# Kernel optimization log

Hardware: AMD Instinct MI355X
Metric: run time of the kernel (lower is better)

Reference implementation:

```python
import jax, jax.numpy as jnp
import numpy as np

HIDDEN_DIM = 2048
NUM_HEADS = 16
HEAD_DIM = HIDDEN_DIM // NUM_HEADS


def setup_inputs() -> dict:
    key = jax.random.key(0)
    k1, k2, k3 = jax.random.split(key, 3)
    x = jax.random.normal(k1, (2, 2048, HIDDEN_DIM), dtype=jnp.float32)
    # nn.Linear weight layout is [out, in]; we store transposed [in, out] for x @ W
    W_qkv = jax.random.normal(k2, (HIDDEN_DIM, 3 * HIDDEN_DIM), dtype=jnp.float32) * (HIDDEN_DIM ** -0.5)
    W_out = jax.random.normal(k3, (HIDDEN_DIM, HIDDEN_DIM), dtype=jnp.float32) * (HIDDEN_DIM ** -0.5)
    return {"x": x, "W_qkv": W_qkv, "W_out": W_out}


def reference(x, W_qkv, W_out):
    B, T, D = x.shape
    H, Hd = NUM_HEADS, HEAD_DIM
    qkv = (x @ W_qkv).reshape(B, T, 3, H, Hd)
    q = qkv[:, :, 0].transpose(0, 2, 1, 3)  # [B,H,T,Hd]
    k = qkv[:, :, 1].transpose(0, 2, 1, 3)
    v = qkv[:, :, 2].transpose(0, 2, 1, 3)
    scale = 1.0 / jnp.sqrt(jnp.asarray(Hd, dtype=x.dtype))
    attn = jnp.einsum('bhqd,bhkd->bhqk', q, k) * scale  # [B,H,T,T]
    causal = jnp.tril(jnp.ones((T, T), dtype=bool))
    attn = jnp.where(causal, attn, jnp.asarray(-jnp.inf, dtype=attn.dtype))
    attn = jax.nn.softmax(attn, axis=-1)
    out = jnp.einsum('bhqk,bhkd->bhqd', attn, v)  # [B,H,T,Hd]
    out = out.transpose(0, 2, 1, 3).reshape(B, T, D)
    return out @ W_out
```

## Files before the change

kernel.cpp:

```cpp
#include <hip/hip_runtime.h>


typedef unsigned short ushort;
typedef __attribute__((ext_vector_type(8))) short short8;
typedef __attribute__((ext_vector_type(4))) float floatx4;

#define T_SEQ 2048
#define NQKV  6144
#define DMODEL 2048
#define HDIM  128
#define NEG_BIG (-3.0e38f)

__device__ __forceinline__ ushort f2bf(float f) {
  unsigned u = __float_as_uint(f);
  u += 0x7fffu + ((u >> 16) & 1u);
  return (ushort)(u >> 16);
}
__device__ __forceinline__ void stout(ushort* p, float v) { *p = f2bf(v); }
__device__ __forceinline__ void stout(float* p, float v)  { *p = v; }

__device__ __forceinline__ void gload_lds16(const ushort* g, ushort* l) {
  __builtin_amdgcn_global_load_lds(
      (const __attribute__((address_space(1))) void*)g,
      (__attribute__((address_space(3))) void*)l,
      16, 0, 0);
}

__global__ void cvt2d(const float* __restrict__ in, ushort* __restrict__ out,
                      int R, int C, int ld_in) {
  int idx = blockIdx.x * blockDim.x + threadIdx.x;
  int c4 = C >> 2;
  if (idx >= R * c4) return;
  int r = idx / c4, c = (idx - r * c4) * 4;
  float4 v = *(const float4*)(in + (size_t)r * ld_in + c);
  ushort4 o;
  o.x = f2bf(v.x); o.y = f2bf(v.y); o.z = f2bf(v.z); o.w = f2bf(v.w);
  *(ushort4*)(out + (size_t)r * C + c) = o;
}

__global__ void cvt2dT(const float* __restrict__ in, ushort* __restrict__ out,
                       int R, int C, int ld_in) {
  __shared__ float tile[32][33];
  int c0 = blockIdx.x * 32, r0 = blockIdx.y * 32;
  int tx = threadIdx.x, ty = threadIdx.y;
#pragma unroll
  for (int q = 0; q < 4; q++)
    tile[ty + q * 8][tx] = in[(size_t)(r0 + ty + q * 8) * ld_in + c0 + tx];
  __syncthreads();
#pragma unroll
  for (int q = 0; q < 4; q++)
    out[(size_t)(c0 + ty + q * 8) * R + r0 + tx] = f2bf(tile[tx][ty + q * 8]);
}

template <typename OutT>
__global__ void gemm_bt(
    const ushort* __restrict__ A, const ushort* __restrict__ Bt,
    OutT* __restrict__ C, int M, int N, int K, int ldc) {
  __shared__ ushort sA[128 * 32];
  __shared__ ushort sB[128 * 32];
  const int tid = threadIdx.x;
  const int w = tid >> 6, l = tid & 63;
  const int quad = l >> 4, l16 = l & 15;
  const int row0 = blockIdx.x * 128, col0 = blockIdx.y * 128;
  const int wm = (w >> 1) * 64, wn = (w & 1) * 64;

  floatx4 acc[4][4];
  const floatx4 zero = {0.f, 0.f, 0.f, 0.f};
#pragma unroll
  for (int i = 0; i < 4; i++)
#pragma unroll
    for (int j = 0; j < 4; j++) acc[i][j] = zero;

  const int srow = w * 16 + (l >> 2);
  const int scol = (l & 3) * 8;
  const ushort* gA = A + (size_t)(row0 + srow) * K + scol;
  const ushort* gB = Bt + (size_t)(col0 + srow) * K + scol;
  ushort* lA = &sA[(w * 16) * 32];
  ushort* lB = &sB[(w * 16) * 32];

  for (int k0 = 0; k0 < K; k0 += 32) {
    __syncthreads();
    gload_lds16(gA + k0, lA);
    gload_lds16(gA + k0 + (size_t)64 * K, lA + 64 * 32);
    gload_lds16(gB + k0, lB);
    gload_lds16(gB + k0 + (size_t)64 * K, lB + 64 * 32);
    __syncthreads();
    short8 af[4], bfr[4];
#pragma unroll
    for (int i = 0; i < 4; i++)
      af[i] = *(const short8*)&sA[(wm + i * 16 + l16) * 32 + quad * 8];
#pragma unroll
    for (int j = 0; j < 4; j++)
      bfr[j] = *(const short8*)&sB[(wn + j * 16 + l16) * 32 + quad * 8];
#pragma unroll
    for (int i = 0; i < 4; i++)
#pragma unroll
      for (int j = 0; j < 4; j++)
        acc[i][j] = __builtin_amdgcn_mfma_f32_16x16x32_bf16(af[i], bfr[j], acc[i][j], 0, 0, 0);
  }

#pragma unroll
  for (int i = 0; i < 4; i++)
#pragma unroll
    for (int j = 0; j < 4; j++) {
      int r0 = row0 + wm + i * 16 + quad * 4;
      int c = col0 + wn + j * 16 + l16;
#pragma unroll
      for (int r = 0; r < 4; r++)
        stout(&C[(size_t)(r0 + r) * ldc + c], acc[i][j][r]);
    }
}

__global__ __launch_bounds__(256, 2) void flash_attn(
    const ushort* __restrict__ qkv, ushort* __restrict__ attn) {
  __shared__ ushort sK[2][16 * 528];
  __shared__ ushort sVt[128 * 72];
  __shared__ ushort sP[4 * 16 * 72];

  const int tid = threadIdx.x;
  const int w = tid >> 6, l = tid & 63;
  const int quad = l >> 4, l16 = l & 15;
  const int bh = blockIdx.x;
  const int qt = 31 - (int)blockIdx.y;
  const int b = bh >> 4, h = bh & 15;
  const size_t rowbase = (size_t)b * T_SEQ;

  short8 qf[4];
  {
    const ushort* qp = qkv + (rowbase + qt * 64 + w * 16 + l16) * NQKV + h * HDIM + quad * 8;
#pragma unroll
    for (int s = 0; s < 4; s++) qf[s] = *(const short8*)(qp + s * 32);
  }
  floatx4 o[8];
  const floatx4 zero = {0.f, 0.f, 0.f, 0.f};
#pragma unroll
  for (int n = 0; n < 8; n++) o[n] = zero;
  float m_i[4], l_i[4];
#pragma unroll
  for (int r = 0; r < 4; r++) { m_i[r] = NEG_BIG; l_i[r] = 0.f; }

  const ushort* gK = qkv + (rowbase + w * 16 + (l >> 4)) * NQKV + 2048 + h * HDIM + (l & 15) * 8;
  auto issueK = [&](int kt, int buf) {
#pragma unroll
    for (int c = 0; c < 4; c++)
      gload_lds16(gK + (size_t)(kt * 64 + c * 4) * NQKV, &sK[buf][(w * 4 + c) * 528]);
  };
  const int v_hd0 = (tid & 15) * 8;
  const int v_t0 = 2 * (tid >> 4);
  const ushort* gV = qkv + rowbase * NQKV + 4096 + h * HDIM + v_hd0;
  short8 vcur[4], vnxt[4];
  auto loadV = [&](int kt, short8* dst) {
#pragma unroll
    for (int c = 0; c < 2; c++) {
      const ushort* g = gV + (size_t)(kt * 64 + v_t0 + 32 * c) * NQKV;
      dst[c] = *(const short8*)g;
      dst[2 + c] = *(const short8*)(g + NQKV);
    }
  };

  ushort* myP = &sP[w * 16 * 72];
  const float scale = 0.08838834764831845f;

  auto attn_step = [&](bool diag, int buf) {
    floatx4 S[4];
#pragma unroll
    for (int j = 0; j < 4; j++) S[j] = zero;
#pragma unroll
    for (int s = 0; s < 4; s++)
#pragma unroll
      for (int j = 0; j < 4; j++) {
        int row = j * 16 + l16;
        short8 kf = *(const short8*)&sK[buf][(row >> 2) * 528 + (row & 3) * 128 + s * 32 + quad * 8];
        S[j] = __builtin_amdgcn_mfma_f32_16x16x32_bf16(qf[s], kf, S[j], 0, 0, 0);
      }
#pragma unroll
    for (int j = 0; j < 4; j++)
#pragma unroll
      for (int r = 0; r < 4; r++) {
        float v = S[j][r] * scale;
        if (diag && (j * 16 + l16 > w * 16 + quad * 4 + r)) v = NEG_BIG;
        S[j][r] = v;
      }
    float alpha[4];
#pragma unroll
    for (int r = 0; r < 4; r++) {
      float v = fmaxf(fmaxf(S[0][r], S[1][r]), fmaxf(S[2][r], S[3][r]));
      v = fmaxf(v, __shfl_xor(v, 1, 16));
      v = fmaxf(v, __shfl_xor(v, 2, 16));
      v = fmaxf(v, __shfl_xor(v, 4, 16));
      v = fmaxf(v, __shfl_xor(v, 8, 16));
      float mn = fmaxf(m_i[r], v);
      alpha[r] = __expf(m_i[r] - mn);
      m_i[r] = mn;
    }
#pragma unroll
    for (int j = 0; j < 4; j++)
#pragma unroll
      for (int r = 0; r < 4; r++) S[j][r] = __expf(S[j][r] - m_i[r]);
#pragma unroll
    for (int r = 0; r < 4; r++)
      l_i[r] = l_i[r] * alpha[r] + S[0][r] + S[1][r] + S[2][r] + S[3][r];
#pragma unroll
    for (int n = 0; n < 8; n++)
#pragma unroll
      for (int r = 0; r < 4; r++) o[n][r] *= alpha[r];
#pragma unroll
    for (int j = 0; j < 4; j++)
#pragma unroll
      for (int r = 0; r < 4; r++)
        myP[(quad * 4 + r) * 72 + j * 16 + l16] = f2bf(S[j][r]);
#pragma unroll
    for (int s = 0; s < 2; s++) {
      short8 pf = *(const short8*)&myP[l16 * 72 + s * 32 + quad * 8];
#pragma unroll
      for (int n = 0; n < 8; n++) {
        int hd = n * 16 + l16;
        short8 vf = *(const short8*)&sVt[hd * 72 + 8 * ((s * 4 + quad) ^ ((hd >> 3) & 7))];
        o[n] = __builtin_amdgcn_mfma_f32_16x16x32_bf16(pf, vf, o[n], 0, 0, 0);
      }
    }
  };

  issueK(0, 0);
  loadV(0, vcur);
  for (int kt = 0; kt <= qt; kt++) {
    const int buf = kt & 1;
    __syncthreads();
#pragma unroll
    for (int c = 0; c < 2; c++) {
      int tw = (v_t0 >> 1) + 16 * c;
#pragma unroll
      for (int j = 0; j < 8; j++) {
        int hd = v_hd0 + j;
        int phys = hd * 72 + 2 * (tw & 3) + 8 * ((tw >> 2) ^ ((hd >> 3) & 7));
        unsigned pv = ((unsigned)(ushort)vcur[c][j]) | (((unsigned)(ushort)vcur[2 + c][j]) << 16);
        *(unsigned*)&sVt[phys] = pv;
      }
    }
    __syncthreads();
    if (kt < qt) {
      issueK(kt + 1, buf ^ 1);
      loadV(kt + 1, vnxt);
    }
    attn_step(kt == qt, buf);
    if (kt < qt) {
#pragma unroll
      for (int c = 0; c < 4; c++) vcur[c] = vnxt[c];
    }
  }

#pragma unroll
  for (int r = 0; r < 4; r++) {
    float v = l_i[r];
    v += __shfl_xor(v, 1, 16);
    v += __shfl_xor(v, 2, 16);
    v += __shfl_xor(v, 4, 16);
    v += __shfl_xor(v, 8, 16);
    l_i[r] = 1.0f / v;
  }
#pragma unroll
  for (int n = 0; n < 8; n++) {
    int col = h * HDIM + n * 16 + l16;
#pragma unroll
    for (int r = 0; r < 4; r++) {
      int row = qt * 64 + w * 16 + quad * 4 + r;
      attn[(rowbase + row) * DMODEL + col] = f2bf(o[n][r] * l_i[r]);
    }
  }
}

extern "C" void kernel_launch(void* const* d_in, const int* in_sizes, int n_in,
                              void* d_out, int out_size, void* d_ws, size_t ws_size,
                              hipStream_t stream) {
  const float* xf    = (const float*)d_in[0];
  const float* Wqkvf = (const float*)d_in[1];
  const float* Woutf = (const float*)d_in[2];
  float* outf = (float*)d_out;
  char* ws = (char*)d_ws;

  const size_t SZ_QKV  = (size_t)4096 * 6144 * 2;
  const size_t SZ_ATTN = (size_t)4096 * 2048 * 2;
  const size_t SZ_WQT  = (size_t)6144 * 2048 * 2;

  ushort* xb = (ushort*)d_out;
  cvt2d<<<8192, 256, 0, stream>>>(xf, xb, 4096, 2048, 2048);

  if (ws_size >= SZ_QKV + SZ_ATTN + SZ_WQT) {
    ushort* qkv   = (ushort*)ws;
    ushort* attnb = (ushort*)(ws + SZ_QKV);
    ushort* WT    = (ushort*)(ws + SZ_QKV + SZ_ATTN);
    cvt2dT<<<dim3(192, 64), dim3(32, 8), 0, stream>>>(Wqkvf, WT, 2048, 6144, NQKV);
    gemm_bt<ushort><<<dim3(32, 48), 256, 0, stream>>>(xb, WT, qkv, 4096, 6144, 2048, NQKV);
    flash_attn<<<dim3(32, 32), 256, 0, stream>>>(qkv, attnb);
    cvt2dT<<<dim3(64, 64), dim3(32, 8), 0, stream>>>(Woutf, WT, 2048, 2048, 2048);
    gemm_bt<float><<<dim3(32, 16), 256, 0, stream>>>(attnb, WT, outf, 4096, 2048, 2048, DMODEL);
  } else {
    ushort* qkv   = (ushort*)ws;
    float*  of    = (float*)ws;
    ushort* wbT   = (ushort*)d_out + (size_t)4096 * 2048;
    ushort* attnb = xb;
    for (int s = 0; s < 3; s++) {
      cvt2dT<<<dim3(64, 64), dim3(32, 8), 0, stream>>>(Wqkvf + s * 2048, wbT, 2048, 2048, NQKV);
      gemm_bt<ushort><<<dim3(32, 16), 256, 0, stream>>>(xb, wbT, qkv + s * 2048, 4096, 2048, 2048, NQKV);
    }
    flash_attn<<<dim3(32, 32), 256, 0, stream>>>(qkv, attnb);
    cvt2dT<<<dim3(64, 64), dim3(32, 8), 0, stream>>>(Woutf, wbT, 2048, 2048, 2048);
    gemm_bt<float><<<dim3(32, 16), 256, 0, stream>>>(attnb, wbT, of, 4096, 2048, 2048, DMODEL);
    hipMemcpyAsync(outf, of, (size_t)4096 * 2048 * 4, hipMemcpyDeviceToDevice, stream);
  }
}
```

Measured before the change: 395.0 us.

## Add 256x256-tile pipelined GEMM with async LDS loads for QKV projection

Adds a new GEMM kernel with 256x256 output tiles, 8 waves per block and direct global-to-LDS loads. It double-buffers K-steps and splits them into phases that interleave the next stage loads with MFMA work, using explicit waitcnt, barriers and setprio. The QKV projection now uses this kernel to raise data reuse per tile and hide load latency. The larger tiles give only 384 blocks and raise register and LDS pressure, and the hand-written waitcnt counts must match the issued loads exactly.

```diff
diff --git a/kernel.cpp b/kernel.cpp
--- a/kernel.cpp
+++ b/kernel.cpp
@@ -10,6 +10,9 @@
 #define DMODEL 2048
 #define HDIM  128
 #define NEG_BIG (-3.0e38f)
+
+#define WAITVM(n) asm volatile("s_waitcnt vmcnt(" #n ")" ::: "memory")
+#define WAITLGKM0 asm volatile("s_waitcnt lgkmcnt(0)" ::: "memory")
 
 __device__ __forceinline__ ushort f2bf(float f) {
   unsigned u = __float_as_uint(f);
@@ -111,6 +114,99 @@
     }
 }
 
+template <typename OutT>
+__global__ __launch_bounds__(512, 2) void gemm_bt_256(
+    const ushort* __restrict__ A, const ushort* __restrict__ Bt,
+    OutT* __restrict__ C, int M, int N, int K, int ldc) {
+  __shared__ ushort sA[2][2][256 * 32];
+  __shared__ ushort sB[2][2][256 * 32];
+  const int tid = threadIdx.x;
+  const int wid = tid >> 6, l = tid & 63;
+  const int quad = l >> 4, l16 = l & 15;
+  const int wr = wid >> 2, wc = wid & 3;
+  const int row0 = blockIdx.x * 256, col0 = blockIdx.y * 256;
+  const int NT = K >> 6;
+
+  floatx4 acc[8][4];
+  const floatx4 zero = {0.f, 0.f, 0.f, 0.f};
+#pragma unroll
+  for (int i = 0; i < 8; i++)
+#pragma unroll
+    for (int j = 0; j < 4; j++) acc[i][j] = zero;
+
+  const ushort* gA = A + (size_t)(row0 + wid * 32 + (l >> 2)) * K + (l & 3) * 8;
+  const ushort* gB = Bt + (size_t)(col0 + wid * 32 + (l >> 2)) * K + (l & 3) * 8;
+
+  auto stageA = [&](int tt, int ks) {
+    ushort* dst = &sA[tt & 1][ks][(wid * 32) * 32];
+    const ushort* g = gA + (size_t)tt * 64 + ks * 32;
+    gload_lds16(g, dst);
+    gload_lds16(g + (size_t)16 * K, dst + 16 * 32);
+  };
+  auto stageB = [&](int tt, int ks) {
+    ushort* dst = &sB[tt & 1][ks][(wid * 32) * 32];
+    const ushort* g = gB + (size_t)tt * 64 + ks * 32;
+    gload_lds16(g, dst);
+    gload_lds16(g + (size_t)16 * K, dst + 16 * 32);
+  };
+
+  stageA(0, 0); stageB(0, 0); stageA(0, 1); stageB(0, 1);
+  if (NT > 1) {
+    stageA(1, 0); stageB(1, 0);
+    WAITVM(4);
+  } else {
+    WAITVM(0);
+  }
+  __builtin_amdgcn_s_barrier();
+
+#define PHASE(ks, ch, STAGE_STMT, VM_TAIL)                                    \
+  {                                                                           \
+    if ((ch) == 0) {                                                          \
+      _Pragma("unroll")                                                       \
+      for (int j = 0; j < 4; j++)                                             \
+        bfr[j] = *(const short8*)&sB[buf][ks][(wc * 64 + j * 16 + l16) * 32 + quad * 8]; \
+    }                                                                         \
+    _Pragma("unroll")                                                         \
+    for (int i = 0; i < 4; i++)                                               \
+      af[i] = *(const short8*)&sA[buf][ks][(wr * 128 + ((ch) * 4 + i) * 16 + l16) * 32 + quad * 8]; \
+    STAGE_STMT;                                                               \
+    __builtin_amdgcn_s_barrier();                                             \
+    WAITLGKM0;                                                                \
+    __builtin_amdgcn_s_setprio(1);                                            \
+    _Pragma("unroll")                                                         \
+    for (int i = 0; i < 4; i++)                                               \
+      _Pragma("unroll")                                                       \
+      for (int j = 0; j < 4; j++)                                             \
+        acc[(ch) * 4 + i][j] = __builtin_amdgcn_mfma_f32_16x16x32_bf16(       \
+            af[i], bfr[j], acc[(ch) * 4 + i][j], 0, 0, 0);                    \
+    __builtin_amdgcn_s_setprio(0);                                            \
+    VM_TAIL;                                                                  \
+    __builtin_amdgcn_s_barrier();                                             \
+  }
+
+  for (int t = 0; t < NT; ++t) {
+    const int buf = t & 1;
+    short8 af[4], bfr[4];
+    PHASE(0, 0, if (t + 1 < NT) stageA(t + 1, 1), );
+    PHASE(0, 1, if (t + 1 < NT) stageB(t + 1, 1), );
+    PHASE(1, 0, if (t + 2 < NT) stageA(t + 2, 0), );
+    PHASE(1, 1, if (t + 2 < NT) stageB(t + 2, 0),
+          if (t < NT - 2) { WAITVM(4); } else if (t == NT - 2) { WAITVM(0); });
+  }
+#undef PHASE
+
+#pragma unroll
+  for (int mi = 0; mi < 8; mi++)
+#pragma unroll
+    for (int j = 0; j < 4; j++) {
+      int r0 = row0 + wr * 128 + mi * 16 + quad * 4;
+      int c = col0 + wc * 64 + j * 16 + l16;
+#pragma unroll
+      for (int r = 0; r < 4; r++)
+        stout(&C[(size_t)(r0 + r) * ldc + c], acc[mi][j][r]);
+    }
+}
+
 __global__ __launch_bounds__(256, 2) void flash_attn(
     const ushort* __restrict__ qkv, ushort* __restrict__ attn) {
   __shared__ ushort sK[2][16 * 528];
@@ -290,7 +386,7 @@
     ushort* attnb = (ushort*)(ws + SZ_QKV);
     ushort* WT    = (ushort*)(ws + SZ_QKV + SZ_ATTN);
     cvt2dT<<<dim3(192, 64), dim3(32, 8), 0, stream>>>(Wqkvf, WT, 2048, 6144, NQKV);
-    gemm_bt<ushort><<<dim3(32, 48), 256, 0, stream>>>(xb, WT, qkv, 4096, 6144, 2048, NQKV);
+    gemm_bt_256<ushort><<<dim3(16, 24), 512, 0, stream>>>(xb, WT, qkv, 4096, 6144, 2048, NQKV);
     flash_attn<<<dim3(32, 32), 256, 0, stream>>>(qkv, attnb);
     cvt2dT<<<dim3(64, 64), dim3(32, 8), 0, stream>>>(Woutf, WT, 2048, 2048, 2048);
     gemm_bt<float><<<dim3(32, 16), 256, 0, stream>>>(attnb, WT, outf, 4096, 2048, 2048, DMODEL);
```

Result: slower. 405.9 us (+2.8%).

## Add 256x384-tile triple-buffered GEMM with 8 waves for QKV projection

Applied to the files above, without the earlier changes.

Replaces the QKV projection GEMM with a new kernel that uses 512 threads, a 256x384 output tile and a three-stage LDS ring filled by direct global-to-LDS loads with an XOR swizzle. Each K step is split into two halves so the next A and B tile loads are issued between MFMA batches, with explicit waitcnt and barrier control and raised wave priority during the MFMA runs. The goal is more operand reuse per LDS byte and better overlap of memory traffic with matrix math. The grid shrinks to 256 blocks, which may underfill the CU count, and each thread now holds 48 accumulators, which raises register pressure.

```diff
diff --git a/kernel.cpp b/kernel.cpp
--- a/kernel.cpp
+++ b/kernel.cpp
@@ -10,6 +10,9 @@
 #define DMODEL 2048
 #define HDIM  128
 #define NEG_BIG (-3.0e38f)
+
+#define WAITVM(n) asm volatile("s_waitcnt vmcnt(" #n ")" ::: "memory")
+#define WAITLGKM0 asm volatile("s_waitcnt lgkmcnt(0)" ::: "memory")
 
 __device__ __forceinline__ ushort f2bf(float f) {
   unsigned u = __float_as_uint(f);
@@ -111,6 +114,104 @@
     }
 }
 
+template <typename OutT>
+__global__ __launch_bounds__(512, 2) void gemm_qkv(
+    const ushort* __restrict__ A, const ushort* __restrict__ Bt,
+    OutT* __restrict__ C, int M, int N, int K, int ldc) {
+  __shared__ ushort sA[3][256 * 32];
+  __shared__ ushort sB[3][384 * 32];
+  const int tid = threadIdx.x;
+  const int wid = tid >> 6, l = tid & 63;
+  const int quad = l >> 4, l16 = l & 15;
+  const int wr = wid >> 2, wc = wid & 3;
+  const int row0 = blockIdx.x * 256, col0 = blockIdx.y * 384;
+  const int NT = K >> 5;
+
+  floatx4 acc[8][6];
+  const floatx4 zero = {0.f, 0.f, 0.f, 0.f};
+#pragma unroll
+  for (int i = 0; i < 8; i++)
+#pragma unroll
+    for (int j = 0; j < 6; j++) acc[i][j] = zero;
+
+  const int sgr = ((l & 3) ^ ((l >> 3) & 3)) * 8;
+  const ushort* gA = A + (size_t)(row0 + wid * 32 + (l >> 2)) * K + sgr;
+  const ushort* gB = Bt + (size_t)(col0 + wid * 48 + (l >> 2)) * K + sgr;
+
+  auto stageA = [&](int tt) {
+    ushort* dst = &sA[tt % 3][(wid * 32) * 32];
+    const ushort* g = gA + tt * 32;
+    gload_lds16(g, dst);
+    gload_lds16(g + (size_t)16 * K, dst + 16 * 32);
+  };
+  auto stageB = [&](int tt) {
+    ushort* dst = &sB[tt % 3][(wid * 48) * 32];
+    const ushort* g = gB + tt * 32;
+    gload_lds16(g, dst);
+    gload_lds16(g + (size_t)16 * K, dst + 16 * 32);
+    gload_lds16(g + (size_t)32 * K, dst + 32 * 32);
+  };
+
+  const int gsw = (quad ^ ((l16 >> 1) & 3)) * 8;
+
+  stageA(0); stageB(0);
+  if (NT > 1) {
+    stageA(1); stageB(1);
+    WAITVM(5);
+  } else {
+    WAITVM(0);
+  }
+  __builtin_amdgcn_s_barrier();
+
+  for (int t = 0; t < NT; ++t) {
+    const int b = t % 3;
+    short8 af[4], bfr[6];
+#pragma unroll
+    for (int j = 0; j < 6; j++)
+      bfr[j] = *(const short8*)&sB[b][(wc * 96 + j * 16 + l16) * 32 + gsw];
+#pragma unroll
+    for (int i = 0; i < 4; i++)
+      af[i] = *(const short8*)&sA[b][(wr * 128 + i * 16 + l16) * 32 + gsw];
+    if (t + 2 < NT) stageA(t + 2);
+    __builtin_amdgcn_s_barrier();
+    WAITLGKM0;
+    __builtin_amdgcn_s_setprio(1);
+#pragma unroll
+    for (int i = 0; i < 4; i++)
+#pragma unroll
+      for (int j = 0; j < 6; j++)
+        acc[i][j] = __builtin_amdgcn_mfma_f32_16x16x32_bf16(af[i], bfr[j], acc[i][j], 0, 0, 0);
+    __builtin_amdgcn_s_setprio(0);
+    __builtin_amdgcn_s_barrier();
+#pragma unroll
+    for (int i = 0; i < 4; i++)
+      af[i] = *(const short8*)&sA[b][(wr * 128 + (4 + i) * 16 + l16) * 32 + gsw];
+    if (t + 2 < NT) stageB(t + 2);
+    __builtin_amdgcn_s_barrier();
+    WAITLGKM0;
+    __builtin_amdgcn_s_setprio(1);
+#pragma unroll
+    for (int i = 0; i < 4; i++)
+#pragma unroll
+      for (int j = 0; j < 6; j++)
+        acc[4 + i][j] = __builtin_amdgcn_mfma_f32_16x16x32_bf16(af[i], bfr[j], acc[4 + i][j], 0, 0, 0);
+    __builtin_amdgcn_s_setprio(0);
+    if (t < NT - 2) { WAITVM(5); } else if (t == NT - 2) { WAITVM(0); }
+    __builtin_amdgcn_s_barrier();
+  }
+
+#pragma unroll
+  for (int mi = 0; mi < 8; mi++)
+#pragma unroll
+    for (int j = 0; j < 6; j++) {
+      int r0 = row0 + wr * 128 + mi * 16 + quad * 4;
+      int c = col0 + wc * 96 + j * 16 + l16;
+#pragma unroll
+      for (int r = 0; r < 4; r++)
+        stout(&C[(size_t)(r0 + r) * ldc + c], acc[mi][j][r]);
+    }
+}
+
 __global__ __launch_bounds__(256, 2) void flash_attn(
     const ushort* __restrict__ qkv, ushort* __restrict__ attn) {
   __shared__ ushort sK[2][16 * 528];
@@ -290,7 +391,7 @@
     ushort* attnb = (ushort*)(ws + SZ_QKV);
     ushort* WT    = (ushort*)(ws + SZ_QKV + SZ_ATTN);
     cvt2dT<<<dim3(192, 64), dim3(32, 8), 0, stream>>>(Wqkvf, WT, 2048, 6144, NQKV);
-    gemm_bt<ushort><<<dim3(32, 48), 256, 0, stream>>>(xb, WT, qkv, 4096, 6144, 2048, NQKV);
+    gemm_qkv<ushort><<<dim3(16, 16), 512, 0, stream>>>(xb, WT, qkv, 4096, 6144, 2048, NQKV);
     flash_attn<<<dim3(32, 32), 256, 0, stream>>>(qkv, attnb);
     cvt2dT<<<dim3(64, 64), dim3(32, 8), 0, stream>>>(Woutf, WT, 2048, 2048, 2048);
     gemm_bt<float><<<dim3(32, 16), 256, 0, stream>>>(attnb, WT, outf, 4096, 2048, 2048, DMODEL);
```

New measurement: 453.1 us. +14.7%, slower.
